# Optimization experiments

Hardware: AMD Instinct MI355X
Metric: run time of the kernel (lower is better)

Reference implementation:

```python
import jax, jax.numpy as jnp
import numpy as np


def setup_inputs() -> dict:
    key = jax.random.key(0)
    ks = jax.random.split(key, 4)
    x = jax.random.normal(ks[0], (1, 896, 1344, 6), dtype=jnp.float32)
    # weights: random_normal init (stddev ~0.05 like keras RandomNormal default), biases zero
    w1 = 0.05 * jax.random.normal(ks[1], (6, 32), dtype=jnp.float32)
    b1 = jnp.zeros((32,), dtype=jnp.float32)
    w2 = 0.05 * jax.random.normal(ks[2], (32, 32), dtype=jnp.float32)
    b2 = jnp.zeros((32,), dtype=jnp.float32)
    w3 = 0.05 * jax.random.normal(ks[3], (32, 3), dtype=jnp.float32)
    b3 = jnp.zeros((3,), dtype=jnp.float32)
    return {"x": x, "w1": w1, "b1": b1, "w2": w2, "b2": b2, "w3": w3, "b3": b3}


def reference(x, w1, b1, w2, b2, w3, b3):
    # The original tiles the image into 448x448 blocks purely as an execution
    # detail; the tiles exactly cover the 896x1344 image, so the math is a
    # per-pixel 3-layer MLP (1x1 conv chain) 6 -> 32 -> 32 -> 3 with relu.
    h1 = jax.nn.relu(jnp.einsum('bhwc,cd->bhwd', x, w1) + b1)   # [1,896,1344,32]
    h2 = jax.nn.relu(jnp.einsum('bhwc,cd->bhwd', h1, w2) + b2)  # [1,896,1344,32]
    out = jax.nn.relu(jnp.einsum('bhwc,cd->bhwd', h2, w3) + b3) # [1,896,1344,3]
    return out
```

## Files before the change

### kernel.cpp

```cpp
#include <hip/hip_runtime.h>

typedef _Float16 f16x8 __attribute__((ext_vector_type(8)));
typedef float    f32x16 __attribute__((ext_vector_type(16)));

#define NPIX (896*1344)
#define TPW   8
#define WPB   4
#define NBLK  (NPIX / (32*TPW*WPB))

__device__ __forceinline__ unsigned pk2(float a, float b) {
    auto h = __builtin_amdgcn_cvt_pkrtz(a, b);
    return __builtin_bit_cast(unsigned, h);
}

__global__ __launch_bounds__(256) void mlp_mfma_kernel(
    const float* __restrict__ x,
    const float* __restrict__ w1, const float* __restrict__ b1,
    const float* __restrict__ w2, const float* __restrict__ b2,
    const float* __restrict__ w3, const float* __restrict__ b3,
    float* __restrict__ out)
{
    __shared__ __align__(16) unsigned lds1[WPB][512];
    __shared__ __align__(16) unsigned lds2[WPB][512];

    const int lane = threadIdx.x & 63;
    const int wv   = threadIdx.x >> 6;
    const int m    = lane & 31;
    const int h    = lane >> 5;
    const int gw   = blockIdx.x * WPB + wv;
    const int swz  = (m >> 1) & 3;

    f16x8 a1, a2f0, a2f1, a3f0, a3f1;
#pragma unroll
    for (int j = 0; j < 8; ++j) {
        int k = 8*h + j;
        float v = w1[(k < 6 ? k : 0)*32 + m];
        a1[j] = (k < 6) ? (_Float16)v : (_Float16)0.0f;
    }
#pragma unroll
    for (int j = 0; j < 8; ++j) a2f0[j] = (_Float16)w2[(8*h + j)*32 + m];
#pragma unroll
    for (int j = 0; j < 8; ++j) a2f1[j] = (_Float16)w2[(16 + 8*h + j)*32 + m];
    const int mc = (m < 3) ? m : 0;
#pragma unroll
    for (int j = 0; j < 8; ++j) {
        float v0 = w3[(8*h + j)*3 + mc];
        float v1 = w3[(16 + 8*h + j)*3 + mc];
        a3f0[j] = (m < 3) ? (_Float16)v0 : (_Float16)0.0f;
        a3f1[j] = (m < 3) ? (_Float16)v1 : (_Float16)0.0f;
    }

    f32x16 bias1, bias2;
#pragma unroll
    for (int r = 0; r < 16; ++r) {
        int row = (r & 3) + 8*(r >> 2) + 4*h;
        bias1[r] = b1[row];
        bias2[r] = b2[row];
    }
    const float b3v0 = b3[0], b3v1 = b3[1], b3v2 = b3[2];

    for (int t = 0; t < TPW; ++t) {
        const int p = gw*(TPW*32) + t*32 + m;

        union { f16x8 v; unsigned u[4]; } bx = {};
        if (h == 0) {
            const float2* xp = (const float2*)(x + (size_t)p*6);
            float2 x01 = xp[0], x23 = xp[1], x45 = xp[2];
            bx.u[0] = pk2(x01.x, x01.y);
            bx.u[1] = pk2(x23.x, x23.y);
            bx.u[2] = pk2(x45.x, x45.y);
        }

        f32x16 acc = __builtin_amdgcn_mfma_f32_32x32x16_f16(a1, bx.v, bias1, 0, 0, 0);
#pragma unroll
        for (int w = 0; w < 4; ++w) {
            unsigned lo = pk2(fmaxf(acc[4*w+0],0.f), fmaxf(acc[4*w+1],0.f));
            unsigned hi = pk2(fmaxf(acc[4*w+2],0.f), fmaxf(acc[4*w+3],0.f));
            int dw = m*16 + 4*(w ^ swz) + 2*h;
            uint2 val; val.x = lo; val.y = hi;
            *(uint2*)&lds1[wv][dw] = val;
        }
        asm volatile("s_waitcnt lgkmcnt(0)" ::: "memory");
        __builtin_amdgcn_sched_barrier(0);

        union { uint4 q; f16x8 v; } bh10, bh11;
        bh10.q = *(const uint4*)&lds1[wv][m*16 + 4*((0 + h) ^ swz)];
        bh11.q = *(const uint4*)&lds1[wv][m*16 + 4*((2 + h) ^ swz)];

        acc = __builtin_amdgcn_mfma_f32_32x32x16_f16(a2f0, bh10.v, bias2, 0, 0, 0);
        acc = __builtin_amdgcn_mfma_f32_32x32x16_f16(a2f1, bh11.v, acc,   0, 0, 0);

#pragma unroll
        for (int w = 0; w < 4; ++w) {
            unsigned lo = pk2(fmaxf(acc[4*w+0],0.f), fmaxf(acc[4*w+1],0.f));
            unsigned hi = pk2(fmaxf(acc[4*w+2],0.f), fmaxf(acc[4*w+3],0.f));
            int dw = m*16 + 4*(w ^ swz) + 2*h;
            uint2 val; val.x = lo; val.y = hi;
            *(uint2*)&lds2[wv][dw] = val;
        }
        asm volatile("s_waitcnt lgkmcnt(0)" ::: "memory");
        __builtin_amdgcn_sched_barrier(0);

        union { uint4 q; f16x8 v; } bh20, bh21;
        bh20.q = *(const uint4*)&lds2[wv][m*16 + 4*((0 + h) ^ swz)];
        bh21.q = *(const uint4*)&lds2[wv][m*16 + 4*((2 + h) ^ swz)];

        f32x16 accz;
#pragma unroll
        for (int r = 0; r < 16; ++r) accz[r] = 0.0f;
        accz = __builtin_amdgcn_mfma_f32_32x32x16_f16(a3f0, bh20.v, accz, 0, 0, 0);
        accz = __builtin_amdgcn_mfma_f32_32x32x16_f16(a3f1, bh21.v, accz, 0, 0, 0);

        if (h == 0) {
            float* op = out + (size_t)p*3;
            op[0] = fmaxf(accz[0] + b3v0, 0.f);
            op[1] = fmaxf(accz[1] + b3v1, 0.f);
            op[2] = fmaxf(accz[2] + b3v2, 0.f);
        }
    }
}

extern "C" void kernel_launch(void* const* d_in, const int* in_sizes, int n_in,
                              void* d_out, int out_size, void* d_ws, size_t ws_size,
                              hipStream_t stream) {
    const float* x  = (const float*)d_in[0];
    const float* w1 = (const float*)d_in[1];
    const float* b1 = (const float*)d_in[2];
    const float* w2 = (const float*)d_in[3];
    const float* b2 = (const float*)d_in[4];
    const float* w3 = (const float*)d_in[5];
    const float* b3 = (const float*)d_in[6];
    float* out = (float*)d_out;

    mlp_mfma_kernel<<<NBLK, 256, 0, stream>>>(x, w1, b1, w2, b2, w3, b3, out);
}
```

Baseline: 97.10 us.

## Replace LDS layer transposes with permlane32 swaps and prefetch next input tile

Moves the MFMA accumulator-to-operand relayout between layers out of LDS and into register lane swaps using permlane32_swap. This removes the shared-memory round trips and waitcnt stalls between layers. It also software-prefetches the next tile's input pixels, folds the layer-3 bias into the MFMA accumulator init, and halves tiles per wave, which doubles the number of blocks. The risks are added register pressure and the correctness of the swap-based fragment layout.

```diff
diff --git a/kernel.cpp b/kernel.cpp
--- a/kernel.cpp
+++ b/kernel.cpp
@@ -4,13 +4,32 @@
 typedef float    f32x16 __attribute__((ext_vector_type(16)));
 
 #define NPIX (896*1344)
-#define TPW   8
+#define TPW   4
 #define WPB   4
 #define NBLK  (NPIX / (32*TPW*WPB))
 
 __device__ __forceinline__ unsigned pk2(float a, float b) {
     auto h = __builtin_amdgcn_cvt_pkrtz(a, b);
     return __builtin_bit_cast(unsigned, h);
+}
+
+__device__ __forceinline__ void pack_swap(const f32x16& acc, f16x8& fr0, f16x8& fr1) {
+    unsigned A0 = pk2(fmaxf(acc[ 0],0.f), fmaxf(acc[ 1],0.f));
+    unsigned A1 = pk2(fmaxf(acc[ 2],0.f), fmaxf(acc[ 3],0.f));
+    unsigned B0 = pk2(fmaxf(acc[ 4],0.f), fmaxf(acc[ 5],0.f));
+    unsigned B1 = pk2(fmaxf(acc[ 6],0.f), fmaxf(acc[ 7],0.f));
+    unsigned C0 = pk2(fmaxf(acc[ 8],0.f), fmaxf(acc[ 9],0.f));
+    unsigned C1 = pk2(fmaxf(acc[10],0.f), fmaxf(acc[11],0.f));
+    unsigned D0 = pk2(fmaxf(acc[12],0.f), fmaxf(acc[13],0.f));
+    unsigned D1 = pk2(fmaxf(acc[14],0.f), fmaxf(acc[15],0.f));
+    auto r0 = __builtin_amdgcn_permlane32_swap(A0, B0, false, false);
+    auto r1 = __builtin_amdgcn_permlane32_swap(A1, B1, false, false);
+    auto r2 = __builtin_amdgcn_permlane32_swap(C0, D0, false, false);
+    auto r3 = __builtin_amdgcn_permlane32_swap(C1, D1, false, false);
+    union { unsigned u[4]; f16x8 v; } u0, u1;
+    u0.u[0] = r0[0]; u0.u[1] = r1[0]; u0.u[2] = r0[1]; u0.u[3] = r1[1];
+    u1.u[0] = r2[0]; u1.u[1] = r3[0]; u1.u[2] = r2[1]; u1.u[3] = r3[1];
+    fr0 = u0.v; fr1 = u1.v;
 }
 
 __global__ __launch_bounds__(256) void mlp_mfma_kernel(
@@ -20,15 +39,11 @@
     const float* __restrict__ w3, const float* __restrict__ b3,
     float* __restrict__ out)
 {
-    __shared__ __align__(16) unsigned lds1[WPB][512];
-    __shared__ __align__(16) unsigned lds2[WPB][512];
-
     const int lane = threadIdx.x & 63;
     const int wv   = threadIdx.x >> 6;
     const int m    = lane & 31;
     const int h    = lane >> 5;
     const int gw   = blockIdx.x * WPB + wv;
-    const int swz  = (m >> 1) & 3;
 
     f16x8 a1, a2f0, a2f1, a3f0, a3f1;
 #pragma unroll
@@ -50,72 +65,52 @@
         a3f1[j] = (m < 3) ? (_Float16)v1 : (_Float16)0.0f;
     }
 
-    f32x16 bias1, bias2;
+    f32x16 bias1, bias2, bias3;
 #pragma unroll
     for (int r = 0; r < 16; ++r) {
         int row = (r & 3) + 8*(r >> 2) + 4*h;
         bias1[r] = b1[row];
         bias2[r] = b2[row];
+        bias3[r] = (h == 0 && r < 3) ? b3[r] : 0.0f;
     }
-    const float b3v0 = b3[0], b3v1 = b3[1], b3v2 = b3[2];
+
+    const float2* xbase = (const float2*)(x + (size_t)(gw*(TPW*32) + m) * 6);
+    float2 nx0, nx1, nx2;
+    if (h == 0) { nx0 = xbase[0]; nx1 = xbase[1]; nx2 = xbase[2]; }
 
     for (int t = 0; t < TPW; ++t) {
         const int p = gw*(TPW*32) + t*32 + m;
 
+        float2 cx0 = nx0, cx1 = nx1, cx2 = nx2;
+        if (h == 0 && t + 1 < TPW) {
+            nx0 = xbase[(t+1)*96 + 0];
+            nx1 = xbase[(t+1)*96 + 1];
+            nx2 = xbase[(t+1)*96 + 2];
+        }
+
         union { f16x8 v; unsigned u[4]; } bx = {};
         if (h == 0) {
-            const float2* xp = (const float2*)(x + (size_t)p*6);
-            float2 x01 = xp[0], x23 = xp[1], x45 = xp[2];
-            bx.u[0] = pk2(x01.x, x01.y);
-            bx.u[1] = pk2(x23.x, x23.y);
-            bx.u[2] = pk2(x45.x, x45.y);
+            bx.u[0] = pk2(cx0.x, cx0.y);
+            bx.u[1] = pk2(cx1.x, cx1.y);
+            bx.u[2] = pk2(cx2.x, cx2.y);
         }
 
         f32x16 acc = __builtin_amdgcn_mfma_f32_32x32x16_f16(a1, bx.v, bias1, 0, 0, 0);
-#pragma unroll
-        for (int w = 0; w < 4; ++w) {
-            unsigned lo = pk2(fmaxf(acc[4*w+0],0.f), fmaxf(acc[4*w+1],0.f));
-            unsigned hi = pk2(fmaxf(acc[4*w+2],0.f), fmaxf(acc[4*w+3],0.f));
-            int dw = m*16 + 4*(w ^ swz) + 2*h;
-            uint2 val; val.x = lo; val.y = hi;
-            *(uint2*)&lds1[wv][dw] = val;
-        }
-        asm volatile("s_waitcnt lgkmcnt(0)" ::: "memory");
-        __builtin_amdgcn_sched_barrier(0);
 
-        union { uint4 q; f16x8 v; } bh10, bh11;
-        bh10.q = *(const uint4*)&lds1[wv][m*16 + 4*((0 + h) ^ swz)];
-        bh11.q = *(const uint4*)&lds1[wv][m*16 + 4*((2 + h) ^ swz)];
+        f16x8 f0, f1;
+        pack_swap(acc, f0, f1);
+        acc = __builtin_amdgcn_mfma_f32_32x32x16_f16(a2f0, f0, bias2, 0, 0, 0);
+        acc = __builtin_amdgcn_mfma_f32_32x32x16_f16(a2f1, f1, acc,   0, 0, 0);
 
-        acc = __builtin_amdgcn_mfma_f32_32x32x16_f16(a2f0, bh10.v, bias2, 0, 0, 0);
-        acc = __builtin_amdgcn_mfma_f32_32x32x16_f16(a2f1, bh11.v, acc,   0, 0, 0);
-
-#pragma unroll
-        for (int w = 0; w < 4; ++w) {
-            unsigned lo = pk2(fmaxf(acc[4*w+0],0.f), fmaxf(acc[4*w+1],0.f));
-            unsigned hi = pk2(fmaxf(acc[4*w+2],0.f), fmaxf(acc[4*w+3],0.f));
-            int dw = m*16 + 4*(w ^ swz) + 2*h;
-            uint2 val; val.x = lo; val.y = hi;
-            *(uint2*)&lds2[wv][dw] = val;
-        }
-        asm volatile("s_waitcnt lgkmcnt(0)" ::: "memory");
-        __builtin_amdgcn_sched_barrier(0);
-
-        union { uint4 q; f16x8 v; } bh20, bh21;
-        bh20.q = *(const uint4*)&lds2[wv][m*16 + 4*((0 + h) ^ swz)];
-        bh21.q = *(const uint4*)&lds2[wv][m*16 + 4*((2 + h) ^ swz)];
-
-        f32x16 accz;
-#pragma unroll
-        for (int r = 0; r < 16; ++r) accz[r] = 0.0f;
-        accz = __builtin_amdgcn_mfma_f32_32x32x16_f16(a3f0, bh20.v, accz, 0, 0, 0);
-        accz = __builtin_amdgcn_mfma_f32_32x32x16_f16(a3f1, bh21.v, accz, 0, 0, 0);
+        pack_swap(acc, f0, f1);
+        f32x16 accz = __builtin_amdgcn_mfma_f32_32x32x16_f16(a3f0, f0, bias3, 0, 0, 0);
+        accz        = __builtin_amdgcn_mfma_f32_32x32x16_f16(a3f1, f1, accz,  0, 0, 0);
 
         if (h == 0) {
             float* op = out + (size_t)p*3;
-            op[0] = fmaxf(accz[0] + b3v0, 0.f);
-            op[1] = fmaxf(accz[1] + b3v1, 0.f);
-            op[2] = fmaxf(accz[2] + b3v2, 0.f);
+            op[0] = fmaxf(accz[0], 0.f);
+            op[1] = fmaxf(accz[1], 0.f);
+            op[2] = fmaxf(accz[2], 0.f);
         }
     }
 }
```

New measurement: 97.06 us. Within noise of the previous version (-0.0%).
